# Kernel tuning notes

Measured on AMD Instinct MI355X. Metric: run time of the kernel, lower is better.

Reference implementation:

```python
import jax, jax.numpy as jnp
import numpy as np

N = 50000      # nodes / stations
E = 600000     # edges
IN = 16        # in_channels
ED = 8         # edge_dim
HID = 128      # hidden
H = 4          # heads
C = HID // H   # 32 per-head channels
EMB = HID // 2 # station embedding dim
FEAT = HID - EMB
SLOPE = 0.2    # GATv2 LeakyReLU negative slope


def setup_inputs() -> dict:
    key = jax.random.key(0)
    ks = jax.random.split(key, 32)
    r = lambda i, shape, s=0.05: (jax.random.normal(ks[i], shape, jnp.float32) * s)
    inp = {
        "x": jax.random.normal(ks[0], (N, IN), jnp.float32),
        "node_idx": jax.random.randint(ks[1], (N,), 0, N),
        "edge_index": jax.random.randint(ks[2], (2, E), 0, N),
        "edge_attr": jax.random.normal(ks[3], (E, ED), jnp.float32),
        # params
        "emb": r(4, (N, EMB)),
        "W_in": r(5, (IN, FEAT)), "b_in": jnp.zeros((FEAT,), jnp.float32),
        # conv1 (GATv2: lin_l, lin_r, lin_edge, att, out bias)
        "Wl1": r(6, (HID, HID)), "bl1": jnp.zeros((HID,), jnp.float32),
        "Wr1": r(7, (HID, HID)), "br1": jnp.zeros((HID,), jnp.float32),
        "We1": r(8, (ED, HID)),  "be1": jnp.zeros((HID,), jnp.float32),
        "att1": r(9, (H, C)),    "bo1": jnp.zeros((HID,), jnp.float32),
        # conv2
        "Wl2": r(10, (HID, HID)), "bl2": jnp.zeros((HID,), jnp.float32),
        "Wr2": r(11, (HID, HID)), "br2": jnp.zeros((HID,), jnp.float32),
        "We2": r(12, (ED, HID)),  "be2": jnp.zeros((HID,), jnp.float32),
        "att2": r(13, (H, C)),    "bo2": jnp.zeros((HID,), jnp.float32),
        # layer norms
        "g1": jnp.ones((HID,), jnp.float32), "beta1": jnp.zeros((HID,), jnp.float32),
        "g2": jnp.ones((HID,), jnp.float32), "beta2": jnp.zeros((HID,), jnp.float32),
        # output head
        "W_out": r(14, (HID, 1)), "b_out": jnp.zeros((1,), jnp.float32),
    }
    return inp


def _gatv2(x, src, dst, ea, Wl, bl, Wr, br, We, be, att, bo):
    # x: [N,HID] -> per-head projections [N,H,C]
    xl = (x @ Wl + bl).reshape(-1, H, C)   # source transform
    xr = (x @ Wr + br).reshape(-1, H, C)   # target transform
    ee = (ea @ We + be).reshape(-1, H, C)  # edge transform [E,H,C]
    s = jax.nn.leaky_relu(xl[src] + xr[dst] + ee, SLOPE)  # [E,H,C]
    logit = jnp.einsum('ehc,hc->eh', s, att)              # [E,H]
    # segment softmax over destination node
    amax = jax.lax.stop_gradient(jax.ops.segment_max(logit, dst, num_segments=N))
    amax = jnp.where(jnp.isfinite(amax), amax, 0.0)
    ex = jnp.exp(logit - amax[dst])
    den = jax.ops.segment_sum(ex, dst, num_segments=N)
    alpha = ex / den[dst]                                  # [E,H]
    out = jax.ops.segment_sum(xl[src] * alpha[..., None], dst, num_segments=N)
    return out.reshape(-1, HID) + bo


def _ln(x, g, b):
    mu = x.mean(-1, keepdims=True)
    v = ((x - mu) ** 2).mean(-1, keepdims=True)
    return (x - mu) * jax.lax.rsqrt(v + 1e-5) * g + b


def reference(x, node_idx, edge_index, edge_attr, emb, W_in, b_in,
              Wl1, bl1, Wr1, br1, We1, be1, att1, bo1,
              Wl2, bl2, Wr2, br2, We2, be2, att2, bo2,
              g1, beta1, g2, beta2, W_out, b_out):
    src, dst = edge_index[0], edge_index[1]
    feat = jax.nn.relu(x @ W_in + b_in)                       # [N,FEAT]
    z = jnp.concatenate([feat, emb[node_idx]], axis=-1)       # [N,HID]
    h = jax.nn.relu(_gatv2(z, src, dst, edge_attr, Wl1, bl1, Wr1, br1, We1, be1, att1, bo1))
    z = _ln(z + h, g1, beta1)
    h = jax.nn.relu(_gatv2(z, src, dst, edge_attr, Wl2, bl2, Wr2, br2, We2, be2, att2, bo2))
    z = _ln(z + h, g2, beta2)
    return (z @ W_out + b_out).squeeze(-1)                    # [N]
```

## Files before the change

kernel.cpp:

```cpp
#include <hip/hip_runtime.h>
#include <hip/hip_bf16.h>

#define NN 50000
#define NE 600000
#define IND 16
#define EDD 8
#define HIDD 128
#define NH 4
#define CC 32
#define EMBD 64
#define FEATD 64
#define NB_SCAN ((NN + 255) / 256)

typedef __hip_bfloat16 bf16;
typedef __attribute__((ext_vector_type(8))) short bshort8;
typedef __attribute__((ext_vector_type(4))) float floatx4;

__device__ __forceinline__ unsigned short f2bu(float f) {
    unsigned int u = __float_as_uint(f);
    u += 0x7fffu + ((u >> 16) & 1u);
    return (unsigned short)(u >> 16);
}

template <bool F32>
__device__ __forceinline__ float LD(const void* p, long long i) {
    if constexpr (F32) return ((const float*)p)[i];
    else return __bfloat162float(((const bf16*)p)[i]);
}

__global__ void k_init0(int* __restrict__ cnt, int* __restrict__ deg, int* __restrict__ dcnt) {
    int i = blockIdx.x * blockDim.x + threadIdx.x;
    if (i == 0) *cnt = 0;
    if (i < NN) deg[i] = 0;
    if (i < 64) dcnt[i] = 0;
}

__global__ void k_detect(const unsigned short* __restrict__ x, int nhalf, int* __restrict__ cnt) {
    __shared__ int c;
    if (threadIdx.x == 0) c = 0;
    __syncthreads();
    int i = blockIdx.x * blockDim.x + threadIdx.x;
    int hits = 0;
    for (; i < nhalf; i += gridDim.x * blockDim.x)
        if ((x[i] & 0x7F80u) == 0x7F80u) hits++;
    if (hits) atomicAdd(&c, hits);
    __syncthreads();
    if (threadIdx.x == 0 && c) atomicAdd(cnt, c);
}

__device__ __forceinline__ bool is_f32(const int* cnt) { return *cnt > 8; }

__global__ void k_hist(const int* __restrict__ ei, int* __restrict__ deg, int* __restrict__ rank) {
    int e = blockIdx.x * blockDim.x + threadIdx.x;
    if (e < NE) rank[e] = atomicAdd(&deg[ei[NE + e]], 1);
}

__global__ void k_scan1(const int* __restrict__ deg, int* __restrict__ off,
                        int* __restrict__ bsum, int* __restrict__ dcnt,
                        int* __restrict__ rankd) {
    __shared__ int tile[256];
    __shared__ int lh[64];
    __shared__ int lbase[64];
    int t = threadIdx.x;
    int gid = blockIdx.x * 256 + t;
    if (t < 64) lh[t] = 0;
    __syncthreads();
    int v = (gid < NN) ? deg[gid] : 0;
    int b = min(v, 63);
    int lr = 0;
    if (gid < NN) lr = atomicAdd(&lh[b], 1);
    tile[t] = v;
    __syncthreads();
    if (t < 64) lbase[t] = lh[t] ? atomicAdd(&dcnt[t], lh[t]) : 0;
    #pragma unroll
    for (int o = 1; o < 256; o <<= 1) {
        int u = (t >= o) ? tile[t - o] : 0;
        __syncthreads();
        tile[t] += u;
        __syncthreads();
    }
    if (gid < NN) {
        off[gid] = tile[t] - v;
        rankd[gid] = lbase[b] + lr;
    }
    if (t == 255) bsum[blockIdx.x] = tile[255];
}
__global__ void k_scan2(int* __restrict__ bsum, int* __restrict__ dcnt,
                        int* __restrict__ dbase) {
    __shared__ int tile[256];
    __shared__ int d2[64];
    int t = threadIdx.x;
    int v = (t < NB_SCAN) ? bsum[t] : 0;
    tile[t] = v;
    int dv = (t < 64) ? dcnt[t] : 0;
    if (t < 64) d2[t] = dv;
    __syncthreads();
    #pragma unroll
    for (int o = 1; o < 256; o <<= 1) {
        int u = (t >= o) ? tile[t - o] : 0;
        __syncthreads();
        tile[t] += u;
        __syncthreads();
    }
    #pragma unroll
    for (int o = 1; o < 64; o <<= 1) {
        int u = (t >= o && t < 64) ? d2[t - o] : 0;
        __syncthreads();
        if (t < 64) d2[t] += u;
        __syncthreads();
    }
    if (t < NB_SCAN) bsum[t] = tile[t] - v;
    if (t < 64) dbase[t] = d2[t] - dv;
}
__global__ void k_scan3(int* __restrict__ off, const int* __restrict__ bsum,
                        const int* __restrict__ deg, const int* __restrict__ rankd,
                        const int* __restrict__ dbase, int* __restrict__ perm) {
    int gid = blockIdx.x * 256 + threadIdx.x;
    if (gid < NN) {
        off[gid] += bsum[blockIdx.x];
        int b = min(deg[gid], 63);
        perm[dbase[b] + rankd[gid]] = gid;
    }
    if (gid == 0) off[NN] = NE;
}

template <bool F32>
__device__ void fill_impl(const int* __restrict__ ei, const int* __restrict__ off,
                          const int* __restrict__ rank, int* __restrict__ esrc,
                          uint4* __restrict__ ea8, const void* ea) {
    int e = blockIdx.x * blockDim.x + threadIdx.x;
    if (e >= NE) return;
    if (e == 0) {
        esrc[NE] = 0;
        uint4 z; z.x = 0; z.y = 0; z.z = 0; z.w = 0;
        ea8[NE] = z;
    }
    int slot = off[ei[NE + e]] + rank[e];
    esrc[slot] = ei[e];
    unsigned int w[4];
    #pragma unroll
    for (int d = 0; d < 4; d++) {
        unsigned int lo = f2bu(LD<F32>(ea, (long long)e * EDD + 2 * d));
        unsigned int hi = f2bu(LD<F32>(ea, (long long)e * EDD + 2 * d + 1));
        w[d] = lo | (hi << 16);
    }
    uint4 v; v.x = w[0]; v.y = w[1]; v.z = w[2]; v.w = w[3];
    ea8[slot] = v;
}
__global__ void k_fill(const int* cnt, const int* ei, const int* off, const int* rank,
                       int* esrc, uint4* ea8, const void* ea) {
    if (is_f32(cnt)) fill_impl<true>(ei, off, rank, esrc, ea8, ea);
    else             fill_impl<false>(ei, off, rank, esrc, ea8, ea);
}

template <bool F32>
__device__ void bzpw_impl(const void* x, const int* __restrict__ node_idx, const void* emb,
                          const void* W_in, const void* b_in, bf16* __restrict__ zb,
                          const void* Wl1, const void* bl1, const void* Wr1, const void* br1,
                          const void* Wl2, const void* bl2, const void* Wr2, const void* br2,
                          bf16* __restrict__ wbT, float* __restrict__ bias) {
    int t = threadIdx.x;
    if (blockIdx.x < NN) {
        int n = blockIdx.x;
        float val;
        if (t < FEATD) {
            float acc = LD<F32>(b_in, t);
            #pragma unroll
            for (int k = 0; k < IND; k++)
                acc += LD<F32>(x, (long long)n * IND + k) * LD<F32>(W_in, k * FEATD + t);
            val = fmaxf(acc, 0.f);
        } else {
            val = LD<F32>(emb, (long long)node_idx[n] * EMBD + (t - FEATD));
        }
        zb[n * HIDD + t] = __float2bfloat16(val);
    } else {
        int bid = blockIdx.x - NN;
        int layer = bid >> 8;
        int n = bid & 255;
        const void* W = layer ? (n < HIDD ? Wl2 : Wr2) : (n < HIDD ? Wl1 : Wr1);
        const void* b = layer ? (n < HIDD ? bl2 : br2) : (n < HIDD ? bl1 : br1);
        int nn = n & (HIDD - 1);
        wbT[(layer * 256 + n) * HIDD + t] = __float2bfloat16(LD<F32>(W, t * HIDD + nn));
        if (t == 0) bias[layer * 256 + n] = LD<F32>(b, nn);
    }
}
__global__ void k_bzpw(const int* cnt, const void* x, const int* node_idx, const void* emb,
                       const void* W_in, const void* b_in, bf16* zb,
                       const void* Wl1, const void* bl1, const void* Wr1, const void* br1,
                       const void* Wl2, const void* bl2, const void* Wr2, const void* br2,
                       bf16* wbT, float* bias) {
    if (is_f32(cnt)) bzpw_impl<true>(x, node_idx, emb, W_in, b_in, zb, Wl1, bl1, Wr1, br1,
                                     Wl2, bl2, Wr2, br2, wbT, bias);
    else             bzpw_impl<false>(x, node_idx, emb, W_in, b_in, zb, Wl1, bl1, Wr1, br1,
                                      Wl2, bl2, Wr2, br2, wbT, bias);
}

__global__ __launch_bounds__(256) void k_projmm(const bf16* __restrict__ zb,
                                                const bf16* __restrict__ wbT,
                                                const float* __restrict__ bias,
                                                bf16* __restrict__ xl, bf16* __restrict__ xr) {
    int wave = threadIdx.x >> 6, lane = threadIdx.x & 63;
    int m0 = blockIdx.x * 32;
    int n0 = wave * 64;
    int l15 = lane & 15, q = lane >> 4;
    bshort8 bfr[4][4];
    #pragma unroll
    for (int j = 0; j < 4; j++)
        #pragma unroll
        for (int s = 0; s < 4; s++)
            bfr[j][s] = *(const bshort8*)(wbT + ((n0 + j * 16 + l15) << 7) + s * 32 + q * 8);
    float bv[4];
    #pragma unroll
    for (int j = 0; j < 4; j++) bv[j] = bias[n0 + j * 16 + l15];
    const bf16* arow0 = zb + ((m0 + l15) << 7) + q * 8;
    const bf16* arow1 = arow0 + (16 << 7);
    bshort8 a0[4], a1[4];
    #pragma unroll
    for (int s = 0; s < 4; s++) a0[s] = *(const bshort8*)(arow0 + s * 32);
    #pragma unroll
    for (int s = 0; s < 4; s++) a1[s] = *(const bshort8*)(arow1 + s * 32);
    #pragma unroll
    for (int mi = 0; mi < 2; mi++) {
        floatx4 acc0 = {0.f, 0.f, 0.f, 0.f}, acc1 = acc0, acc2 = acc0, acc3 = acc0;
        #pragma unroll
        for (int s = 0; s < 4; s++) {
            bshort8 a = mi ? a1[s] : a0[s];
            acc0 = __builtin_amdgcn_mfma_f32_16x16x32_bf16(a, bfr[0][s], acc0, 0, 0, 0);
            acc1 = __builtin_amdgcn_mfma_f32_16x16x32_bf16(a, bfr[1][s], acc1, 0, 0, 0);
            acc2 = __builtin_amdgcn_mfma_f32_16x16x32_bf16(a, bfr[2][s], acc2, 0, 0, 0);
            acc3 = __builtin_amdgcn_mfma_f32_16x16x32_bf16(a, bfr[3][s], acc3, 0, 0, 0);
        }
        floatx4 accs[4] = {acc0, acc1, acc2, acc3};
        #pragma unroll
        for (int j = 0; j < 4; j++) {
            int colg = n0 + j * 16 + l15;
            bf16* dst = (colg < HIDD) ? (xl + colg) : (xr + (colg - HIDD));
            #pragma unroll
            for (int r = 0; r < 4; r++) {
                int rowc = m0 + mi * 16 + q * 4 + r;
                if (rowc < NN) dst[rowc << 7] = __float2bfloat16(accs[j][r] + bv[j]);
            }
        }
    }
}

template <bool F32, bool LAST>
__device__ void gat_impl(const int* __restrict__ perm,
                         const int* __restrict__ off, const int* __restrict__ esrc,
                         const uint4* __restrict__ ea8,
                         const void* We, const void* be, const void* att,
                         const bf16* __restrict__ xl, const bf16* __restrict__ xr,
                         const void* bo, bf16* __restrict__ zb,
                         const void* g, const void* beta,
                         const void* Wo, const void* bout, void* out) {
    int wave = threadIdx.x >> 6;
    int half = (threadIdx.x >> 5) & 1;
    int lane5 = threadIdx.x & 31;
    int n = perm[blockIdx.x * 8 + wave * 2 + half];
    int c0 = lane5 << 2;
    float wv[EDD][4], at[4], bev[4];
    #pragma unroll
    for (int d = 0; d < EDD; d++)
        #pragma unroll
        for (int j = 0; j < 4; j++) wv[d][j] = LD<F32>(We, d * HIDD + c0 + j);
    #pragma unroll
    for (int j = 0; j < 4; j++) {
        at[j] = LD<F32>(att, c0 + j);
        bev[j] = LD<F32>(be, c0 + j);
    }
    uint2 xru = *(const uint2*)(xr + (n << 7) + c0);
    float xrv[4];
    xrv[0] = __uint_as_float(xru.x << 16);
    xrv[1] = __uint_as_float(xru.x & 0xffff0000u);
    xrv[2] = __uint_as_float(xru.y << 16);
    xrv[3] = __uint_as_float(xru.y & 0xffff0000u);
    int lo = off[n], hi = off[n + 1];
    float acc[4] = {0.f, 0.f, 0.f, 0.f};
    float den = 0.f;
    if (lo < hi) {
        int src = esrc[lo];
        uint4 eu = ea8[lo];
        uint2 xu = *(const uint2*)(xl + (src << 7) + c0);
        for (int i = lo; i < hi; i++) {
            int src_n = esrc[i + 1];
            uint4 eu_n = ea8[i + 1];
            uint2 xu_n = *(const uint2*)(xl + (src_n << 7) + c0);
            float e[8];
            e[0] = __uint_as_float(eu.x << 16); e[1] = __uint_as_float(eu.x & 0xffff0000u);
            e[2] = __uint_as_float(eu.y << 16); e[3] = __uint_as_float(eu.y & 0xffff0000u);
            e[4] = __uint_as_float(eu.z << 16); e[5] = __uint_as_float(eu.z & 0xffff0000u);
            e[6] = __uint_as_float(eu.w << 16); e[7] = __uint_as_float(eu.w & 0xffff0000u);
            float xv[4];
            xv[0] = __uint_as_float(xu.x << 16);
            xv[1] = __uint_as_float(xu.x & 0xffff0000u);
            xv[2] = __uint_as_float(xu.y << 16);
            xv[3] = __uint_as_float(xu.y & 0xffff0000u);
            float ls = 0.f;
            #pragma unroll
            for (int j = 0; j < 4; j++) {
                float ee = bev[j];
                #pragma unroll
                for (int d = 0; d < EDD; d++) ee += e[d] * wv[d][j];
                float s = xv[j] + xrv[j] + ee;
                s = fmaxf(s, 0.2f * s);
                ls += s * at[j];
            }
            ls += __shfl_xor(ls, 1);
            ls += __shfl_xor(ls, 2);
            ls += __shfl_xor(ls, 4);
            float ex = __expf(ls);
            #pragma unroll
            for (int j = 0; j < 4; j++) acc[j] += ex * xv[j];
            den += ex;
            src = src_n; eu = eu_n; xu = xu_n;
        }
    }
    float inv = (den > 0.f) ? 1.0f / den : 0.f;
    uint2 zu = *(const uint2*)(zb + (n << 7) + c0);
    float zv[4];
    zv[0] = __uint_as_float(zu.x << 16);
    zv[1] = __uint_as_float(zu.x & 0xffff0000u);
    zv[2] = __uint_as_float(zu.y << 16);
    zv[3] = __uint_as_float(zu.y & 0xffff0000u);
    float v[4];
    float s = 0.f;
    #pragma unroll
    for (int j = 0; j < 4; j++) {
        float hv = fmaxf(acc[j] * inv + LD<F32>(bo, c0 + j), 0.f);
        v[j] = zv[j] + hv;
        s += v[j];
    }
    #pragma unroll
    for (int m = 16; m; m >>= 1) s += __shfl_xor(s, m);
    float mu = s * (1.f / HIDD);
    float s2 = 0.f;
    float dv[4];
    #pragma unroll
    for (int j = 0; j < 4; j++) { dv[j] = v[j] - mu; s2 += dv[j] * dv[j]; }
    #pragma unroll
    for (int m = 16; m; m >>= 1) s2 += __shfl_xor(s2, m);
    float rs = rsqrtf(s2 * (1.f / HIDD) + 1e-5f);
    float o[4];
    #pragma unroll
    for (int j = 0; j < 4; j++)
        o[j] = dv[j] * rs * LD<F32>(g, c0 + j) + LD<F32>(beta, c0 + j);
    if constexpr (!LAST) {
        uint2 pk;
        pk.x = (unsigned int)f2bu(o[0]) | ((unsigned int)f2bu(o[1]) << 16);
        pk.y = (unsigned int)f2bu(o[2]) | ((unsigned int)f2bu(o[3]) << 16);
        *(uint2*)(zb + (n << 7) + c0) = pk;
    } else {
        float po = 0.f;
        #pragma unroll
        for (int j = 0; j < 4; j++) po += o[j] * LD<F32>(Wo, c0 + j);
        #pragma unroll
        for (int m = 16; m; m >>= 1) po += __shfl_xor(po, m);
        if (lane5 == 0) {
            float r = po + LD<F32>(bout, 0);
            if constexpr (F32) ((float*)out)[n] = r;
            else               ((bf16*)out)[n] = __float2bfloat16(r);
        }
    }
}
__global__ void k_gat(const int* cnt, const int* perm, const int* off, const int* esrc,
                      const uint4* ea8, const void* We, const void* be, const void* att,
                      const bf16* xl, const bf16* xr, const void* bo, bf16* zb,
                      const void* g, const void* beta) {
    if (is_f32(cnt)) gat_impl<true, false>(perm, off, esrc, ea8, We, be, att, xl, xr, bo, zb, g, beta, nullptr, nullptr, nullptr);
    else             gat_impl<false, false>(perm, off, esrc, ea8, We, be, att, xl, xr, bo, zb, g, beta, nullptr, nullptr, nullptr);
}
__global__ void k_gat_last(const int* cnt, const int* perm, const int* off, const int* esrc,
                           const uint4* ea8, const void* We, const void* be, const void* att,
                           const bf16* xl, const bf16* xr, const void* bo, bf16* zb,
                           const void* g, const void* beta,
                           const void* Wo, const void* bout, void* out) {
    if (is_f32(cnt)) gat_impl<true, true>(perm, off, esrc, ea8, We, be, att, xl, xr, bo, zb, g, beta, Wo, bout, out);
    else             gat_impl<false, true>(perm, off, esrc, ea8, We, be, att, xl, xr, bo, zb, g, beta, Wo, bout, out);
}

extern "C" void kernel_launch(void* const* d_in, const int* in_sizes, int n_in,
                              void* d_out, int out_size, void* d_ws, size_t ws_size,
                              hipStream_t stream) {
    const void* x        = d_in[0];
    const int*  node_idx = (const int*)d_in[1];
    const int*  ei       = (const int*)d_in[2];
    const void* ea       = d_in[3];
    const void* emb      = d_in[4];
    const void* W_in     = d_in[5];
    const void* b_in     = d_in[6];
    const void* Wl1 = d_in[7];  const void* bl1 = d_in[8];
    const void* Wr1 = d_in[9];  const void* br1 = d_in[10];
    const void* We1 = d_in[11]; const void* be1 = d_in[12];
    const void* att1 = d_in[13]; const void* bo1 = d_in[14];
    const void* Wl2 = d_in[15]; const void* bl2 = d_in[16];
    const void* Wr2 = d_in[17]; const void* br2 = d_in[18];
    const void* We2 = d_in[19]; const void* be2 = d_in[20];
    const void* att2 = d_in[21]; const void* bo2 = d_in[22];
    const void* g1 = d_in[23]; const void* beta1 = d_in[24];
    const void* g2 = d_in[25]; const void* beta2 = d_in[26];
    const void* W_out = d_in[27]; const void* b_out = d_in[28];

    int*   cnt   = (int*)d_ws;
    uint4* ea8   = (uint4*)((char*)d_ws + 256);
    bf16*  zb    = (bf16*)(ea8 + NE + 4);
    bf16*  xl    = zb + NN * HIDD;
    bf16*  xr    = xl + NN * HIDD;
    bf16*  wbT   = xr + NN * HIDD;
    float* bias  = (float*)(wbT + 2 * 256 * HIDD);
    int*   off   = (int*)(bias + 512);
    int*   deg   = off + NN + 1;
    int*   rank  = deg + NN;
    int*   rankd = rank + NE;
    int*   perm  = rankd + NN;
    int*   esrc  = perm + NN;
    int*   bsum  = esrc + NE + 4;
    int*   dcnt  = bsum + 256;
    int*   dbase = dcnt + 64;

    int nhalf = in_sizes[0] < 65536 ? in_sizes[0] : 65536;
    k_init0<<<(NN + 255) / 256, 256, 0, stream>>>(cnt, deg, dcnt);
    k_detect<<<64, 256, 0, stream>>>((const unsigned short*)x, nhalf, cnt);
    k_bzpw<<<NN + 512, HIDD, 0, stream>>>(cnt, x, node_idx, emb, W_in, b_in, zb,
                                          Wl1, bl1, Wr1, br1, Wl2, bl2, Wr2, br2, wbT, bias);

    k_hist<<<(NE + 255) / 256, 256, 0, stream>>>(ei, deg, rank);
    k_scan1<<<NB_SCAN, 256, 0, stream>>>(deg, off, bsum, dcnt, rankd);
    k_scan2<<<1, 256, 0, stream>>>(bsum, dcnt, dbase);
    k_scan3<<<NB_SCAN, 256, 0, stream>>>(off, bsum, deg, rankd, dbase, perm);
    k_fill<<<(NE + 255) / 256, 256, 0, stream>>>(cnt, ei, off, rank, esrc, ea8, ea);

    k_projmm<<<(NN + 31) / 32, 256, 0, stream>>>(zb, wbT, bias, xl, xr);
    k_gat<<<NN / 8, 256, 0, stream>>>(cnt, perm, off, esrc, ea8, We1, be1, att1, xl, xr, bo1, zb, g1, beta1);

    k_projmm<<<(NN + 31) / 32, 256, 0, stream>>>(zb, wbT + 256 * HIDD, bias + 256, xl, xr);
    k_gat_last<<<NN / 8, 256, 0, stream>>>(cnt, perm, off, esrc, ea8, We2, be2, att2, xl, xr, bo2, zb,
                                           g2, beta2, W_out, b_out, d_out);
}
```

Measured before the change: 408.9 us.

## Unroll GAT edge loop by two, merge detect/init kernels, reorder launches

```diff
diff --git a/kernel.cpp b/kernel.cpp
--- a/kernel.cpp
+++ b/kernel.cpp
@@ -28,27 +28,29 @@
     else return __bfloat162float(((const bf16*)p)[i]);
 }
 
-__global__ void k_init0(int* __restrict__ cnt, int* __restrict__ deg, int* __restrict__ dcnt) {
-    int i = blockIdx.x * blockDim.x + threadIdx.x;
-    if (i == 0) *cnt = 0;
-    if (i < NN) deg[i] = 0;
-    if (i < 64) dcnt[i] = 0;
-}
-
-__global__ void k_detect(const unsigned short* __restrict__ x, int nhalf, int* __restrict__ cnt) {
-    __shared__ int c;
-    if (threadIdx.x == 0) c = 0;
-    __syncthreads();
-    int i = blockIdx.x * blockDim.x + threadIdx.x;
-    int hits = 0;
-    for (; i < nhalf; i += gridDim.x * blockDim.x)
-        if ((x[i] & 0x7F80u) == 0x7F80u) hits++;
-    if (hits) atomicAdd(&c, hits);
-    __syncthreads();
-    if (threadIdx.x == 0 && c) atomicAdd(cnt, c);
-}
-
 __device__ __forceinline__ bool is_f32(const int* cnt) { return *cnt > 8; }
+
+__global__ void k_detinit(const unsigned short* __restrict__ x, int nhalf,
+                          int* __restrict__ cnt, int* __restrict__ deg,
+                          int* __restrict__ dcnt) {
+    if (blockIdx.x == 0) {
+        __shared__ int red[256];
+        int hits = 0;
+        for (int i = threadIdx.x; i < nhalf; i += 256)
+            if ((x[i] & 0x7F80u) == 0x7F80u) hits++;
+        red[threadIdx.x] = hits;
+        __syncthreads();
+        for (int o = 128; o; o >>= 1) {
+            if (threadIdx.x < o) red[threadIdx.x] += red[threadIdx.x + o];
+            __syncthreads();
+        }
+        if (threadIdx.x == 0) *cnt = red[0];
+    } else {
+        int gid = (blockIdx.x - 1) * 256 + threadIdx.x;
+        if (gid < NN) deg[gid] = 0;
+        if (blockIdx.x == 1 && threadIdx.x < 64) dcnt[threadIdx.x] = 0;
+    }
+}
 
 __global__ void k_hist(const int* __restrict__ ei, int* __restrict__ deg, int* __restrict__ rank) {
     int e = blockIdx.x * blockDim.x + threadIdx.x;
@@ -130,10 +132,10 @@
                           uint4* __restrict__ ea8, const void* ea) {
     int e = blockIdx.x * blockDim.x + threadIdx.x;
     if (e >= NE) return;
-    if (e == 0) {
-        esrc[NE] = 0;
+    if (e < 6) {
+        esrc[NE + e] = 0;
         uint4 z; z.x = 0; z.y = 0; z.z = 0; z.w = 0;
-        ea8[NE] = z;
+        ea8[NE + e] = z;
     }
     int slot = off[ei[NE + e]] + rank[e];
     esrc[slot] = ei[e];
@@ -244,6 +246,37 @@
     }
 }
 
+__device__ __forceinline__ void edge_body(uint4 eu, uint2 xu, const float (*wv)[4],
+                                          const float* bev, const float* at,
+                                          const float* xrv, float mask,
+                                          float* acc, float& den) {
+    float e[8];
+    e[0] = __uint_as_float(eu.x << 16); e[1] = __uint_as_float(eu.x & 0xffff0000u);
+    e[2] = __uint_as_float(eu.y << 16); e[3] = __uint_as_float(eu.y & 0xffff0000u);
+    e[4] = __uint_as_float(eu.z << 16); e[5] = __uint_as_float(eu.z & 0xffff0000u);
+    e[6] = __uint_as_float(eu.w << 16); e[7] = __uint_as_float(eu.w & 0xffff0000u);
+    float xv[4];
+    xv[0] = __uint_as_float(xu.x << 16); xv[1] = __uint_as_float(xu.x & 0xffff0000u);
+    xv[2] = __uint_as_float(xu.y << 16); xv[3] = __uint_as_float(xu.y & 0xffff0000u);
+    float ls = 0.f;
+    #pragma unroll
+    for (int j = 0; j < 4; j++) {
+        float ee = bev[j];
+        #pragma unroll
+        for (int d = 0; d < EDD; d++) ee += e[d] * wv[d][j];
+        float s = xv[j] + xrv[j] + ee;
+        s = fmaxf(s, 0.2f * s);
+        ls += s * at[j];
+    }
+    ls += __shfl_xor(ls, 1);
+    ls += __shfl_xor(ls, 2);
+    ls += __shfl_xor(ls, 4);
+    float ex = __expf(ls) * mask;
+    #pragma unroll
+    for (int j = 0; j < 4; j++) acc[j] += ex * xv[j];
+    den += ex;
+}
+
 template <bool F32, bool LAST>
 __device__ void gat_impl(const int* __restrict__ perm,
                          const int* __restrict__ off, const int* __restrict__ esrc,
@@ -275,47 +308,31 @@
     xrv[2] = __uint_as_float(xru.y << 16);
     xrv[3] = __uint_as_float(xru.y & 0xffff0000u);
     int lo = off[n], hi = off[n + 1];
-    float acc[4] = {0.f, 0.f, 0.f, 0.f};
-    float den = 0.f;
+    float accA[4] = {0.f, 0.f, 0.f, 0.f}, accB[4] = {0.f, 0.f, 0.f, 0.f};
+    float denA = 0.f, denB = 0.f;
     if (lo < hi) {
-        int src = esrc[lo];
-        uint4 eu = ea8[lo];
-        uint2 xu = *(const uint2*)(xl + (src << 7) + c0);
-        for (int i = lo; i < hi; i++) {
-            int src_n = esrc[i + 1];
-            uint4 eu_n = ea8[i + 1];
-            uint2 xu_n = *(const uint2*)(xl + (src_n << 7) + c0);
-            float e[8];
-            e[0] = __uint_as_float(eu.x << 16); e[1] = __uint_as_float(eu.x & 0xffff0000u);
-            e[2] = __uint_as_float(eu.y << 16); e[3] = __uint_as_float(eu.y & 0xffff0000u);
-            e[4] = __uint_as_float(eu.z << 16); e[5] = __uint_as_float(eu.z & 0xffff0000u);
-            e[6] = __uint_as_float(eu.w << 16); e[7] = __uint_as_float(eu.w & 0xffff0000u);
-            float xv[4];
-            xv[0] = __uint_as_float(xu.x << 16);
-            xv[1] = __uint_as_float(xu.x & 0xffff0000u);
-            xv[2] = __uint_as_float(xu.y << 16);
-            xv[3] = __uint_as_float(xu.y & 0xffff0000u);
-            float ls = 0.f;
-            #pragma unroll
-            for (int j = 0; j < 4; j++) {
-                float ee = bev[j];
-                #pragma unroll
-                for (int d = 0; d < EDD; d++) ee += e[d] * wv[d][j];
-                float s = xv[j] + xrv[j] + ee;
-                s = fmaxf(s, 0.2f * s);
-                ls += s * at[j];
-            }
-            ls += __shfl_xor(ls, 1);
-            ls += __shfl_xor(ls, 2);
-            ls += __shfl_xor(ls, 4);
-            float ex = __expf(ls);
-            #pragma unroll
-            for (int j = 0; j < 4; j++) acc[j] += ex * xv[j];
-            den += ex;
-            src = src_n; eu = eu_n; xu = xu_n;
-        }
-    }
-    float inv = (den > 0.f) ? 1.0f / den : 0.f;
+        int sA = esrc[lo],      sB = esrc[lo + 1];
+        uint4 eA = ea8[lo],     eB = ea8[lo + 1];
+        uint2 xA = *(const uint2*)(xl + (sA << 7) + c0);
+        uint2 xB = *(const uint2*)(xl + (sB << 7) + c0);
+        int snA = esrc[lo + 2], snB = esrc[lo + 3];
+        uint4 enA = ea8[lo + 2], enB = ea8[lo + 3];
+        for (int i = lo; i < hi; i += 2) {
+            uint2 xnA = *(const uint2*)(xl + (snA << 7) + c0);
+            uint2 xnB = *(const uint2*)(xl + (snB << 7) + c0);
+            int s2A = esrc[i + 4],  s2B = esrc[i + 5];
+            uint4 e2A = ea8[i + 4], e2B = ea8[i + 5];
+            edge_body(eA, xA, wv, bev, at, xrv, 1.f, accA, denA);
+            float mB = (i + 1 < hi) ? 1.f : 0.f;
+            edge_body(eB, xB, wv, bev, at, xrv, mB, accB, denB);
+            eA = enA; eB = enB; xA = xnA; xB = xnB;
+            snA = s2A; snB = s2B; enA = e2A; enB = e2B;
+        }
+        #pragma unroll
+        for (int j = 0; j < 4; j++) accA[j] += accB[j];
+        denA += denB;
+    }
+    float inv = (denA > 0.f) ? 1.0f / denA : 0.f;
     uint2 zu = *(const uint2*)(zb + (n << 7) + c0);
     float zv[4];
     zv[0] = __uint_as_float(zu.x << 16);
@@ -326,7 +343,7 @@
     float s = 0.f;
     #pragma unroll
     for (int j = 0; j < 4; j++) {
-        float hv = fmaxf(acc[j] * inv + LD<F32>(bo, c0 + j), 0.f);
+        float hv = fmaxf(accA[j] * inv + LD<F32>(bo, c0 + j), 0.f);
         v[j] = zv[j] + hv;
         s += v[j];
     }
@@ -402,7 +419,7 @@
 
     int*   cnt   = (int*)d_ws;
     uint4* ea8   = (uint4*)((char*)d_ws + 256);
-    bf16*  zb    = (bf16*)(ea8 + NE + 4);
+    bf16*  zb    = (bf16*)(ea8 + NE + 8);
     bf16*  xl    = zb + NN * HIDD;
     bf16*  xr    = xl + NN * HIDD;
     bf16*  wbT   = xr + NN * HIDD;
@@ -413,20 +430,18 @@
     int*   rankd = rank + NE;
     int*   perm  = rankd + NN;
     int*   esrc  = perm + NN;
-    int*   bsum  = esrc + NE + 4;
+    int*   bsum  = esrc + NE + 8;
     int*   dcnt  = bsum + 256;
     int*   dbase = dcnt + 64;
 
-    int nhalf = in_sizes[0] < 65536 ? in_sizes[0] : 65536;
-    k_init0<<<(NN + 255) / 256, 256, 0, stream>>>(cnt, deg, dcnt);
-    k_detect<<<64, 256, 0, stream>>>((const unsigned short*)x, nhalf, cnt);
-    k_bzpw<<<NN + 512, HIDD, 0, stream>>>(cnt, x, node_idx, emb, W_in, b_in, zb,
-                                          Wl1, bl1, Wr1, br1, Wl2, bl2, Wr2, br2, wbT, bias);
-
+    int nhalf = in_sizes[0] < 16384 ? in_sizes[0] : 16384;
+    k_detinit<<<NB_SCAN + 1, 256, 0, stream>>>((const unsigned short*)x, nhalf, cnt, deg, dcnt);
     k_hist<<<(NE + 255) / 256, 256, 0, stream>>>(ei, deg, rank);
     k_scan1<<<NB_SCAN, 256, 0, stream>>>(deg, off, bsum, dcnt, rankd);
     k_scan2<<<1, 256, 0, stream>>>(bsum, dcnt, dbase);
     k_scan3<<<NB_SCAN, 256, 0, stream>>>(off, bsum, deg, rankd, dbase, perm);
+    k_bzpw<<<NN + 512, HIDD, 0, stream>>>(cnt, x, node_idx, emb, W_in, b_in, zb,
+                                          Wl1, bl1, Wr1, br1, Wl2, bl2, Wr2, br2, wbT, bias);
     k_fill<<<(NE + 255) / 256, 256, 0, stream>>>(cnt, ei, off, rank, esrc, ea8, ea);
 
     k_projmm<<<(NN + 31) / 32, 256, 0, stream>>>(zb, wbT, bias, xl, xr);
```

Result: no change. 403.1 us (median of 2 runs) (-1.4%).
